# Performance work log

Hardware: AMD Instinct MI355X
Metric: run time of the kernel (lower is better)

The kernel has to match this reference:

```python
import jax, jax.numpy as jnp
import numpy as np

N_HEADS = 16
ROPE_BASE = 10000.0

def _rope_cos_sin(seq_len, head_dim):
    # freqs[t, j] = t / base**(2j/head_dim), j over head_dim//2 pairs
    inv_freq = 1.0 / (ROPE_BASE ** (jnp.arange(0, head_dim, 2, dtype=jnp.float32) / head_dim))
    t = jnp.arange(seq_len, dtype=jnp.float32)
    freqs = t[:, None] * inv_freq[None, :]          # [S, hd/2]
    return jnp.cos(freqs), jnp.sin(freqs)

def _apply_rope(x, cos, sin):
    # x: [B, S, H, hd]; pairs are interleaved (even, odd) -> complex (re, im)
    xr = x[..., 0::2]
    xi = x[..., 1::2]
    c = cos[None, :, None, :]
    s = sin[None, :, None, :]
    out_r = xr * c - xi * s
    out_i = xr * s + xi * c
    # interleave back: [..., hd/2, 2] -> [..., hd]
    return jnp.stack([out_r, out_i], axis=-1).reshape(x.shape)

def setup_inputs() -> dict:
    key = jax.random.key(0)
    ks = jax.random.split(key, 5)
    B, S, D = 2, 2048, 2048
    x = jax.random.normal(ks[0], (B, S, D), dtype=jnp.float32)
    w_scale = 0.02
    wq = jax.random.normal(ks[1], (D, D), dtype=jnp.float32) * w_scale
    wk = jax.random.normal(ks[2], (D, D), dtype=jnp.float32) * w_scale
    wv = jax.random.normal(ks[3], (D, D), dtype=jnp.float32) * w_scale
    wo = jax.random.normal(ks[4], (D, D), dtype=jnp.float32) * w_scale
    return {"x": x, "wq": wq, "wk": wk, "wv": wv, "wo": wo}

def reference(x, wq, wk, wv, wo):
    B, S, D = x.shape
    H = N_HEADS
    hd = D // H
    # QKV projections (torch Linear: y = x @ W^T)
    q = (x @ wq.T).reshape(B, S, H, hd)
    k = (x @ wk.T).reshape(B, S, H, hd)
    v = (x @ wv.T).reshape(B, S, H, hd)
    cos, sin = _rope_cos_sin(S, hd)
    q = _apply_rope(q, cos, sin)
    k = _apply_rope(k, cos, sin)
    # -> [B, H, S, hd]
    q = q.transpose(0, 2, 1, 3)
    k = k.transpose(0, 2, 1, 3)
    v = v.transpose(0, 2, 1, 3)
    scale = 1.0 / jnp.sqrt(jnp.float32(hd))
    scores = jnp.einsum('bhqd,bhkd->bhqk', q, k) * scale
    causal = jnp.tril(jnp.ones((S, S), dtype=bool))
    scores = jnp.where(causal[None, None], scores, jnp.float32(-1e30))
    probs = jax.nn.softmax(scores, axis=-1)
    attn = jnp.einsum('bhqk,bhkd->bhqd', probs, v)  # [B, H, S, hd]
    attn = attn.transpose(0, 2, 1, 3).reshape(B, S, D)
    return attn @ wo.T
```

## Files before the change

### kernel.cpp

```cpp
#include <hip/hip_runtime.h>
#include <hip/hip_bf16.h>

using bf16 = __hip_bfloat16;
typedef __attribute__((ext_vector_type(8))) short short8;
typedef __attribute__((ext_vector_type(4))) float floatx4;
typedef __attribute__((ext_vector_type(2))) float floatx2;

#define GLDS16(g, l)                                                        \
  __builtin_amdgcn_global_load_lds(                                         \
      (const __attribute__((address_space(1))) void*)(g),                   \
      (__attribute__((address_space(3))) void*)(l), 16, 0, 0)

#define MFMA16(a, b, c) __builtin_amdgcn_mfma_f32_16x16x32_bf16(a, b, c, 0, 0, 0)

__device__ __forceinline__ short f2b(float x) {
  union { bf16 h; short s; } u;
  u.h = __float2bfloat16(x);
  return u.s;
}
__device__ __forceinline__ void st(float* p, float v) { *p = v; }
__device__ __forceinline__ void st(bf16* p, float v) { *p = __float2bfloat16(v); }

template <int CTRL>
__device__ __forceinline__ float dpp_f(float x) {
  return __int_as_float(__builtin_amdgcn_update_dpp(
      0, __float_as_int(x), CTRL, 0xF, 0xF, true));
}
__device__ __forceinline__ float red16_max(float x) {
  x = fmaxf(x, dpp_f<0xB1>(x));
  x = fmaxf(x, dpp_f<0x4E>(x));
  x = fmaxf(x, dpp_f<0x141>(x));
  x = fmaxf(x, dpp_f<0x140>(x));
  return x;
}
__device__ __forceinline__ float red16_sum(float x) {
  x += dpp_f<0xB1>(x);
  x += dpp_f<0x4E>(x);
  x += dpp_f<0x141>(x);
  x += dpp_f<0x140>(x);
  return x;
}

__global__ void cast_kernel(const float* __restrict__ in, bf16* __restrict__ out,
                            long n) {
  long i = ((long)blockIdx.x * blockDim.x + threadIdx.x) * 8;
  if (i >= n) return;
  floatx4 a = *(const floatx4*)(in + i);
  floatx4 b = *(const floatx4*)(in + i + 4);
  short8 r;
  r[0] = f2b(a[0]); r[1] = f2b(a[1]); r[2] = f2b(a[2]); r[3] = f2b(a[3]);
  r[4] = f2b(b[0]); r[5] = f2b(b[1]); r[6] = f2b(b[2]); r[7] = f2b(b[3]);
  *(short8*)(out + i) = r;
}

__global__ void rope_tab_kernel(floatx2* __restrict__ tab) {
  const int t = blockIdx.x * blockDim.x + threadIdx.x;
  const int s = t >> 6, p = t & 63;
  const float invf = exp2f(-(float)p * (13.287712379549449f / 64.0f));
  float sn, cs;
  sincosf((float)s * invf, &sn, &cs);
  floatx2 e; e[0] = cs; e[1] = sn;
  tab[t] = e;
}

__device__ __forceinline__ void gemm_core(
    const bf16* __restrict__ A, const bf16* __restrict__ B, int K,
    long m0, long n0, bf16* As, bf16* Bs, floatx4 (&acc)[8][4])
{
  const int tid  = threadIdx.x;
  const int wave = tid >> 6;
  const int lane = tid & 63;
  const int quad = lane >> 4;
  const int l16  = lane & 15;
  const int wr = wave >> 1;
  const int wc = wave & 1;

  long ga[4];
  int aoff[4];
#pragma unroll
  for (int i = 0; i < 4; i++) {
    const int c = i * 256 + tid;
    const int row = c >> 2;
    const int gch = (c & 3) ^ ((c >> 3) & 3);
    ga[i] = (m0 + row) * (long)K + gch * 8;
    aoff[i] = (i * 256 + wave * 64) * 8;
  }
  long gb[2];
  int boff[2];
#pragma unroll
  for (int i = 0; i < 2; i++) {
    const int c = i * 256 + tid;
    const int row = c >> 2;
    const int gch = (c & 3) ^ ((c >> 3) & 3);
    gb[i] = (n0 + row) * (long)K + gch * 8;
    boff[i] = (i * 256 + wave * 64) * 8;
  }

  const int qs = (quad ^ ((l16 >> 1) & 3)) * 8;

#pragma unroll
  for (int mi = 0; mi < 8; mi++)
#pragma unroll
    for (int ni = 0; ni < 4; ni++) {
      floatx4 z = {0.f, 0.f, 0.f, 0.f};
      acc[mi][ni] = z;
    }

  const int NT = K >> 5;

#pragma unroll
  for (int t = 0; t < 2; t++) {
    bf16* Ad = As + t * 8192;
    bf16* Bd = Bs + t * 4096;
    const long kk = (long)t * 32;
#pragma unroll
    for (int i = 0; i < 4; i++) GLDS16(A + ga[i] + kk, Ad + aoff[i]);
#pragma unroll
    for (int i = 0; i < 2; i++) GLDS16(B + gb[i] + kk, Bd + boff[i]);
  }

  int sl = 0;
  for (int t = 0; t < NT; t++) {
    if (t < NT - 1) asm volatile("s_waitcnt vmcnt(6)" ::: "memory");
    else            asm volatile("s_waitcnt vmcnt(0)" ::: "memory");
    __builtin_amdgcn_s_barrier();

    const bf16* Ab = As + sl * 8192;
    const bf16* Bb = Bs + sl * 4096;

    short8 a[8], b[4];
#pragma unroll
    for (int mi = 0; mi < 8; mi++)
      a[mi] = *(const short8*)(Ab + (wr * 128 + mi * 16 + l16) * 32 + qs);
#pragma unroll
    for (int ni = 0; ni < 4; ni++)
      b[ni] = *(const short8*)(Bb + (wc * 64 + ni * 16 + l16) * 32 + qs);

    if (t + 2 < NT) {
      int s2 = sl + 2; if (s2 >= 3) s2 -= 3;
      bf16* Ad = As + s2 * 8192;
      bf16* Bd = Bs + s2 * 4096;
      const long kk = (long)(t + 2) * 32;
#pragma unroll
      for (int i = 0; i < 4; i++) GLDS16(A + ga[i] + kk, Ad + aoff[i]);
#pragma unroll
      for (int i = 0; i < 2; i++) GLDS16(B + gb[i] + kk, Bd + boff[i]);
    }

    asm volatile("s_waitcnt lgkmcnt(0)" ::: "memory");
    __builtin_amdgcn_sched_barrier(0);
    __builtin_amdgcn_s_setprio(1);
#pragma unroll
    for (int mi = 0; mi < 8; mi++)
#pragma unroll
      for (int ni = 0; ni < 4; ni++)
        acc[mi][ni] = MFMA16(a[mi], b[ni], acc[mi][ni]);
    __builtin_amdgcn_s_setprio(0);

    sl++; if (sl >= 3) sl = 0;
  }
}

__global__ __launch_bounds__(256, 2) void qkv_gemm(
    const bf16* __restrict__ A,
    const bf16* __restrict__ B0, const bf16* __restrict__ B1,
    const bf16* __restrict__ B2,
    bf16* __restrict__ C0, bf16* __restrict__ C1, bf16* __restrict__ Cvt,
    const floatx2* __restrict__ rtab,
    int M, int N, int K)
{
  __shared__ __align__(16) bf16 As[3 * 8192];
  __shared__ __align__(16) bf16 Bs[3 * 4096];

  const int sel = blockIdx.y >> 4;
  const long m0 = (long)blockIdx.x * 256;
  const long n0 = (long)(blockIdx.y & 15) * 128;
  const bf16* B = (sel == 0) ? B0 : ((sel == 1) ? B1 : B2);

  floatx4 acc[8][4];
  gemm_core(A, B, K, m0, n0, As, Bs, acc);

  const int tid  = threadIdx.x;
  const int wave = tid >> 6;
  const int lane = tid & 63;
  const int quad = lane >> 4;
  const int l16  = lane & 15;
  const int wr = wave >> 1;
  const int wc = wave & 1;

  if (sel < 2) {
    bf16* C = (sel == 0) ? C0 : C1;
    const float qscale = (sel == 0)
        ? (0.08838834764831845f * 1.4426950408889634f) : 1.0f;
    const float sgn = (l16 & 1) ? 1.0f : -1.0f;
#pragma unroll
    for (int ni = 0; ni < 4; ni++) {
      const int n = (int)n0 + wc * 64 + ni * 16 + l16;
      const int p = (n & 127) >> 1;
#pragma unroll
      for (int mi = 0; mi < 8; mi++) {
        floatx4 v = acc[mi][ni];
        const int mbase = (int)m0 + wr * 128 + mi * 16 + quad * 4;
#pragma unroll
        for (int r = 0; r < 4; r++) {
          const int spos = (mbase + r) & 2047;
          const floatx2 cssn = rtab[spos * 64 + p];
          const float pv = dpp_f<0xB1>(v[r]);
          const float outv = (v[r] * cssn[0] + pv * (sgn * cssn[1])) * qscale;
          st(&C[(long)(mbase + r) * N + n], outv);
        }
      }
    }
  } else {
#pragma unroll
    for (int ni = 0; ni < 4; ni++) {
      const int n = (int)n0 + wc * 64 + ni * 16 + l16;
      const int hh = n >> 7, d = n & 127;
#pragma unroll
      for (int mi = 0; mi < 8; mi++) {
        floatx4 v = acc[mi][ni];
        const int m = (int)m0 + wr * 128 + mi * 16 + quad * 4;
        const int bb = m >> 11, s = m & 2047;
        unsigned long long pk =
            (unsigned long long)(unsigned short)f2b(v[0]) |
            ((unsigned long long)(unsigned short)f2b(v[1]) << 16) |
            ((unsigned long long)(unsigned short)f2b(v[2]) << 32) |
            ((unsigned long long)(unsigned short)f2b(v[3]) << 48);
        *(unsigned long long*)(Cvt + ((long)((bb * 16 + hh) * 128 + d)) * 2048 + s) = pk;
      }
    }
  }
}

__global__ __launch_bounds__(256, 2) void gemm_out(
    const bf16* __restrict__ A, const bf16* __restrict__ B,
    float* __restrict__ C, int M, int N, int K)
{
  __shared__ __align__(16) bf16 As[3 * 8192];
  __shared__ __align__(16) bf16 Bs[3 * 4096];
  const long m0 = (long)blockIdx.x * 256;
  const long n0 = (long)blockIdx.y * 128;

  floatx4 acc[8][4];
  gemm_core(A, B, K, m0, n0, As, Bs, acc);

  const int tid  = threadIdx.x;
  const int wave = tid >> 6;
  const int lane = tid & 63;
  const int quad = lane >> 4;
  const int l16  = lane & 15;
  const int wr = wave >> 1;
  const int wc = wave & 1;

#pragma unroll
  for (int mi = 0; mi < 8; mi++)
#pragma unroll
    for (int ni = 0; ni < 4; ni++) {
      floatx4 v = acc[mi][ni];
      const long row = m0 + wr * 128 + mi * 16 + quad * 4;
      const long col = n0 + wc * 64 + ni * 16 + l16;
#pragma unroll
      for (int r = 0; r < 4; r++)
        C[(row + r) * (long)N + col] = v[r];
    }
}

#define NEG_BIG (-30000.0f)

__global__ __launch_bounds__(256) void flash_attn(
    const bf16* __restrict__ q, const bf16* __restrict__ k,
    const bf16* __restrict__ vt, bf16* __restrict__ o, int S)
{
  __shared__ bf16 Ks[64 * 136];
  __shared__ bf16 Vt[128 * 72];
  __shared__ bf16 Ps[4][32 * 72];

  const int tid  = threadIdx.x;
  const int wave = tid >> 6;
  const int lane = tid & 63;
  const int quad = lane >> 4;
  const int l16  = lane & 15;

  const int bh = blockIdx.x;
  const int b  = bh >> 4, h = bh & 15;
  const int q0 = ((int)gridDim.y - 1 - (int)blockIdx.y) * 128;

  const bf16* Qb = q + ((long)b * S * 16 + h) * 128;
  const bf16* Kb = k + ((long)b * S * 16 + h) * 128;
  const bf16* Vg = vt + (long)bh * 128 * S;
  bf16*       Ob = o + ((long)b * S * 16 + h) * 128;

  int kr[4], kc[4], vr[4], vc[4];
#pragma unroll
  for (int it = 0; it < 4; it++) {
    const int c = tid + it * 256;
    kr[it] = c >> 4;  kc[it] = (c & 15) * 8;
    vr[it] = c >> 3;  vc[it] = (c & 7) * 8;
  }

  short8 aq[2][4];
#pragma unroll
  for (int mi = 0; mi < 2; mi++)
#pragma unroll
    for (int kt = 0; kt < 4; kt++)
      aq[mi][kt] = *(const short8*)(
          Qb + (long)(q0 + wave * 32 + mi * 16 + l16) * 2048 + kt * 32 + quad * 8);

  float m_i[2][4], l_i[2][4];
  floatx4 oacc[2][8];
  const floatx4 zero4 = {0.f, 0.f, 0.f, 0.f};
#pragma unroll
  for (int mi = 0; mi < 2; mi++) {
#pragma unroll
    for (int r = 0; r < 4; r++) { m_i[mi][r] = NEG_BIG; l_i[mi][r] = 0.f; }
#pragma unroll
    for (int dt = 0; dt < 8; dt++) oacc[mi][dt] = zero4;
  }

  const int wrow0 = q0 + wave * 32;
  const int last  = q0 + 64;

  short8 kreg[4], vreg[4];
#pragma unroll
  for (int it = 0; it < 4; it++) {
    kreg[it] = *(const short8*)(Kb + (long)kr[it] * 2048 + kc[it]);
    vreg[it] = *(const short8*)(Vg + (long)vr[it] * S + vc[it]);
  }

  for (int kt0 = 0; kt0 <= last; kt0 += 64) {
    __syncthreads();

#pragma unroll
    for (int it = 0; it < 4; it++) {
      *(short8*)(Ks + kr[it] * 136 + kc[it]) = kreg[it];
      *(short8*)(Vt + vr[it] * 72 + vc[it]) = vreg[it];
    }
    __syncthreads();

    if (kt0 < last) {
      const int n0 = kt0 + 64;
#pragma unroll
      for (int it = 0; it < 4; it++) {
        kreg[it] = *(const short8*)(Kb + (long)(n0 + kr[it]) * 2048 + kc[it]);
        vreg[it] = *(const short8*)(Vg + (long)vr[it] * S + n0 + vc[it]);
      }
    }

    if (kt0 <= wrow0 + 31) {
      floatx4 sc[2][4];
#pragma unroll
      for (int mi = 0; mi < 2; mi++)
#pragma unroll
        for (int nt = 0; nt < 4; nt++) sc[mi][nt] = zero4;

      __builtin_amdgcn_s_setprio(1);
#pragma unroll
      for (int nt = 0; nt < 4; nt++)
#pragma unroll
        for (int kt = 0; kt < 4; kt++) {
          short8 bk = *(const short8*)(Ks + (nt * 16 + l16) * 136 + kt * 32 + quad * 8);
          sc[0][nt] = __builtin_amdgcn_mfma_f32_16x16x32_bf16(aq[0][kt], bk, sc[0][nt], 0, 0, 0);
          sc[1][nt] = __builtin_amdgcn_mfma_f32_16x16x32_bf16(aq[1][kt], bk, sc[1][nt], 0, 0, 0);
        }
      __builtin_amdgcn_s_setprio(0);

      const bool needmask = (kt0 + 63 > wrow0);
      float mx[2][4];
      int allskip = 1;
#pragma unroll
      for (int mi = 0; mi < 2; mi++) {
#pragma unroll
        for (int r = 0; r < 4; r++) {
          const int qr = wrow0 + mi * 16 + quad * 4 + r;
          float m = NEG_BIG;
          if (needmask) {
#pragma unroll
            for (int nt = 0; nt < 4; nt++) {
              const int kc2 = kt0 + nt * 16 + l16;
              float vsc = (kc2 <= qr) ? sc[mi][nt][r] : NEG_BIG;
              sc[mi][nt][r] = vsc;
              m = fmaxf(m, vsc);
            }
          } else {
#pragma unroll
            for (int nt = 0; nt < 4; nt++) m = fmaxf(m, sc[mi][nt][r]);
          }
          m = red16_max(m);
          mx[mi][r] = m;
          allskip &= (m <= m_i[mi][r] + 8.0f) ? 1 : 0;
        }
      }

      if (!__all(allskip)) {
#pragma unroll
        for (int mi = 0; mi < 2; mi++) {
#pragma unroll
          for (int r = 0; r < 4; r++) {
            const float mnew = fmaxf(m_i[mi][r], mx[mi][r]);
            const float alpha = exp2f(m_i[mi][r] - mnew);
            m_i[mi][r] = mnew;
            l_i[mi][r] *= alpha;
#pragma unroll
            for (int dt = 0; dt < 8; dt++) oacc[mi][dt][r] *= alpha;
          }
        }
      }

#pragma unroll
      for (int mi = 0; mi < 2; mi++) {
#pragma unroll
        for (int r = 0; r < 4; r++) {
          float rs = 0.f;
#pragma unroll
          for (int nt = 0; nt < 4; nt++) {
            float p = exp2f(sc[mi][nt][r] - m_i[mi][r]);
            sc[mi][nt][r] = p;
            rs += p;
          }
          rs = red16_sum(rs);
          l_i[mi][r] += rs;
        }
      }

#pragma unroll
      for (int mi = 0; mi < 2; mi++)
#pragma unroll
        for (int nt = 0; nt < 4; nt++)
#pragma unroll
          for (int r = 0; r < 4; r++)
            Ps[wave][(mi * 16 + quad * 4 + r) * 72 + nt * 16 + l16] =
                __float2bfloat16(sc[mi][nt][r]);

      __builtin_amdgcn_s_setprio(1);
#pragma unroll
      for (int ks = 0; ks < 2; ks++) {
        short8 ap0 = *(const short8*)(&Ps[wave][(l16) * 72 + ks * 32 + quad * 8]);
        short8 ap1 = *(const short8*)(&Ps[wave][(16 + l16) * 72 + ks * 32 + quad * 8]);
#pragma unroll
        for (int dt = 0; dt < 8; dt++) {
          short8 bv = *(const short8*)(Vt + (dt * 16 + l16) * 72 + ks * 32 + quad * 8);
          oacc[0][dt] = __builtin_amdgcn_mfma_f32_16x16x32_bf16(ap0, bv, oacc[0][dt], 0, 0, 0);
          oacc[1][dt] = __builtin_amdgcn_mfma_f32_16x16x32_bf16(ap1, bv, oacc[1][dt], 0, 0, 0);
        }
      }
      __builtin_amdgcn_s_setprio(0);
    }
  }

#pragma unroll
  for (int mi = 0; mi < 2; mi++)
#pragma unroll
    for (int r = 0; r < 4; r++) {
      const float inv = 1.0f / l_i[mi][r];
      const long s = q0 + wave * 32 + mi * 16 + quad * 4 + r;
#pragma unroll
      for (int dt = 0; dt < 8; dt++)
        Ob[s * 2048 + dt * 16 + l16] = __float2bfloat16(oacc[mi][dt][r] * inv);
    }
}

extern "C" void kernel_launch(void* const* d_in, const int* in_sizes, int n_in,
                              void* d_out, int out_size, void* d_ws, size_t ws_size,
                              hipStream_t stream) {
  const float* x  = (const float*)d_in[0];
  const float* wq = (const float*)d_in[1];
  const float* wk = (const float*)d_in[2];
  const float* wv = (const float*)d_in[3];
  const float* wo = (const float*)d_in[4];
  float* out = (float*)d_out;

  const int B = 2, S = 2048, D = 2048, H = 16;
  const int M = B * S;
  const long tsz = (long)M * D;
  const long wsz = (long)D * D;

  if (ws_size < 4 * (size_t)tsz * sizeof(bf16)) return;

  bf16* qb  = (bf16*)d_ws;
  bf16* kb  = qb + tsz;
  bf16* vtb = kb + tsz;
  bf16* ab  = vtb + tsz;

  bf16* xb  = (bf16*)d_out;
  bf16* wqb = xb + tsz;
  bf16* wkb = wqb + wsz;
  bf16* wvb = ab;
  floatx2* rtab = (floatx2*)(ab + wsz);
  bf16* wob = qb;

  cast_kernel<<<(int)(tsz / 8 / 256), 256, 0, stream>>>(x,  xb,  tsz);
  cast_kernel<<<(int)(wsz / 8 / 256), 256, 0, stream>>>(wq, wqb, wsz);
  cast_kernel<<<(int)(wsz / 8 / 256), 256, 0, stream>>>(wk, wkb, wsz);
  cast_kernel<<<(int)(wsz / 8 / 256), 256, 0, stream>>>(wv, wvb, wsz);
  rope_tab_kernel<<<(S * 64) / 256, 256, 0, stream>>>(rtab);

  qkv_gemm<<<dim3(16, 48), 256, 0, stream>>>(
      xb, wqb, wkb, wvb, qb, kb, vtb, rtab, M, D, D);

  flash_attn<<<dim3(B * H, S / 128), 256, 0, stream>>>(qb, kb, vtb, ab, S);

  cast_kernel<<<(int)(wsz / 8 / 256), 256, 0, stream>>>(wo, wob, wsz);
  gemm_out<<<dim3(16, 16), 256, 0, stream>>>(ab, wob, out, M, D, D);
}
```

Before: 417.3 us.

## Fuse pre-casts and rope table into one launch; drop LDS staging in attention

```diff
diff --git a/kernel.cpp b/kernel.cpp
--- a/kernel.cpp
+++ b/kernel.cpp
@@ -39,6 +39,45 @@
   x += dpp_f<0x141>(x);
   x += dpp_f<0x140>(x);
   return x;
+}
+
+__global__ void fused_pre(const float* __restrict__ x,
+                          const float* __restrict__ wq,
+                          const float* __restrict__ wk,
+                          const float* __restrict__ wv,
+                          bf16* __restrict__ xb, bf16* __restrict__ wqb,
+                          bf16* __restrict__ wkb, bf16* __restrict__ wvb,
+                          floatx2* __restrict__ rtab, long wsz) {
+  const int slice = blockIdx.y;
+  if (slice == 5) {
+    const int t = blockIdx.x * blockDim.x + threadIdx.x;
+    if (t < 131072) {
+      const int s = t >> 6, p = t & 63;
+      const float invf = exp2f(-(float)p * (13.287712379549449f / 64.0f));
+      float sn, cs;
+      sincosf((float)s * invf, &sn, &cs);
+      floatx2 e; e[0] = cs; e[1] = sn;
+      rtab[t] = e;
+    }
+    return;
+  }
+  const float* src;
+  bf16* dst;
+  switch (slice) {
+    case 0:  src = x;        dst = xb;        break;
+    case 1:  src = x + wsz;  dst = xb + wsz;  break;
+    case 2:  src = wq;       dst = wqb;       break;
+    case 3:  src = wk;       dst = wkb;       break;
+    default: src = wv;       dst = wvb;       break;
+  }
+  const long i = ((long)blockIdx.x * blockDim.x + threadIdx.x) * 8;
+  if (i >= wsz) return;
+  floatx4 a = *(const floatx4*)(src + i);
+  floatx4 b = *(const floatx4*)(src + i + 4);
+  short8 r;
+  r[0] = f2b(a[0]); r[1] = f2b(a[1]); r[2] = f2b(a[2]); r[3] = f2b(a[3]);
+  r[4] = f2b(b[0]); r[5] = f2b(b[1]); r[6] = f2b(b[2]); r[7] = f2b(b[3]);
+  *(short8*)(dst + i) = r;
 }
 
 __global__ void cast_kernel(const float* __restrict__ in, bf16* __restrict__ out,
@@ -51,16 +90,6 @@
   r[0] = f2b(a[0]); r[1] = f2b(a[1]); r[2] = f2b(a[2]); r[3] = f2b(a[3]);
   r[4] = f2b(b[0]); r[5] = f2b(b[1]); r[6] = f2b(b[2]); r[7] = f2b(b[3]);
   *(short8*)(out + i) = r;
-}
-
-__global__ void rope_tab_kernel(floatx2* __restrict__ tab) {
-  const int t = blockIdx.x * blockDim.x + threadIdx.x;
-  const int s = t >> 6, p = t & 63;
-  const float invf = exp2f(-(float)p * (13.287712379549449f / 64.0f));
-  float sn, cs;
-  sincosf((float)s * invf, &sn, &cs);
-  floatx2 e; e[0] = cs; e[1] = sn;
-  tab[t] = e;
 }
 
 __device__ __forceinline__ void gemm_core(
@@ -271,8 +300,6 @@
     const bf16* __restrict__ q, const bf16* __restrict__ k,
     const bf16* __restrict__ vt, bf16* __restrict__ o, int S)
 {
-  __shared__ bf16 Ks[64 * 136];
-  __shared__ bf16 Vt[128 * 72];
   __shared__ bf16 Ps[4][32 * 72];
 
   const int tid  = threadIdx.x;
@@ -290,14 +317,6 @@
   const bf16* Vg = vt + (long)bh * 128 * S;
   bf16*       Ob = o + ((long)b * S * 16 + h) * 128;
 
-  int kr[4], kc[4], vr[4], vc[4];
-#pragma unroll
-  for (int it = 0; it < 4; it++) {
-    const int c = tid + it * 256;
-    kr[it] = c >> 4;  kc[it] = (c & 15) * 8;
-    vr[it] = c >> 3;  vc[it] = (c & 7) * 8;
-  }
-
   short8 aq[2][4];
 #pragma unroll
   for (int mi = 0; mi < 2; mi++)
@@ -318,133 +337,108 @@
   }
 
   const int wrow0 = q0 + wave * 32;
-  const int last  = q0 + 64;
-
-  short8 kreg[4], vreg[4];
-#pragma unroll
-  for (int it = 0; it < 4; it++) {
-    kreg[it] = *(const short8*)(Kb + (long)kr[it] * 2048 + kc[it]);
-    vreg[it] = *(const short8*)(Vg + (long)vr[it] * S + vc[it]);
-  }
-
-  for (int kt0 = 0; kt0 <= last; kt0 += 64) {
-    __syncthreads();
-
-#pragma unroll
-    for (int it = 0; it < 4; it++) {
-      *(short8*)(Ks + kr[it] * 136 + kc[it]) = kreg[it];
-      *(short8*)(Vt + vr[it] * 72 + vc[it]) = vreg[it];
-    }
-    __syncthreads();
-
-    if (kt0 < last) {
-      const int n0 = kt0 + 64;
-#pragma unroll
-      for (int it = 0; it < 4; it++) {
-        kreg[it] = *(const short8*)(Kb + (long)(n0 + kr[it]) * 2048 + kc[it]);
-        vreg[it] = *(const short8*)(Vg + (long)vr[it] * S + n0 + vc[it]);
-      }
-    }
-
-    if (kt0 <= wrow0 + 31) {
-      floatx4 sc[2][4];
-#pragma unroll
-      for (int mi = 0; mi < 2; mi++)
-#pragma unroll
-        for (int nt = 0; nt < 4; nt++) sc[mi][nt] = zero4;
-
-      __builtin_amdgcn_s_setprio(1);
+  const int wlast = wrow0 + 31;
+
+  for (int kt0 = 0; kt0 <= wlast; kt0 += 64) {
+    floatx4 sc[2][4];
+#pragma unroll
+    for (int mi = 0; mi < 2; mi++)
+#pragma unroll
+      for (int nt = 0; nt < 4; nt++) sc[mi][nt] = zero4;
+
+    __builtin_amdgcn_s_setprio(1);
+#pragma unroll
+    for (int nt = 0; nt < 4; nt++)
+#pragma unroll
+      for (int kt = 0; kt < 4; kt++) {
+        short8 bk = *(const short8*)(
+            Kb + (long)(kt0 + nt * 16 + l16) * 2048 + kt * 32 + quad * 8);
+        sc[0][nt] = __builtin_amdgcn_mfma_f32_16x16x32_bf16(aq[0][kt], bk, sc[0][nt], 0, 0, 0);
+        sc[1][nt] = __builtin_amdgcn_mfma_f32_16x16x32_bf16(aq[1][kt], bk, sc[1][nt], 0, 0, 0);
+      }
+    __builtin_amdgcn_s_setprio(0);
+
+    const bool needmask = (kt0 + 63 > wrow0);
+    float mx[2][4];
+    int allskip = 1;
+#pragma unroll
+    for (int mi = 0; mi < 2; mi++) {
+#pragma unroll
+      for (int r = 0; r < 4; r++) {
+        const int qr = wrow0 + mi * 16 + quad * 4 + r;
+        float m = NEG_BIG;
+        if (needmask) {
+#pragma unroll
+          for (int nt = 0; nt < 4; nt++) {
+            const int kc2 = kt0 + nt * 16 + l16;
+            float vsc = (kc2 <= qr) ? sc[mi][nt][r] : NEG_BIG;
+            sc[mi][nt][r] = vsc;
+            m = fmaxf(m, vsc);
+          }
+        } else {
+#pragma unroll
+          for (int nt = 0; nt < 4; nt++) m = fmaxf(m, sc[mi][nt][r]);
+        }
+        m = red16_max(m);
+        mx[mi][r] = m;
+        allskip &= (m <= m_i[mi][r] + 8.0f) ? 1 : 0;
+      }
+    }
+
+    if (!__all(allskip)) {
+#pragma unroll
+      for (int mi = 0; mi < 2; mi++) {
+#pragma unroll
+        for (int r = 0; r < 4; r++) {
+          const float mnew = fmaxf(m_i[mi][r], mx[mi][r]);
+          const float alpha = exp2f(m_i[mi][r] - mnew);
+          m_i[mi][r] = mnew;
+          l_i[mi][r] *= alpha;
+#pragma unroll
+          for (int dt = 0; dt < 8; dt++) oacc[mi][dt][r] *= alpha;
+        }
+      }
+    }
+
+#pragma unroll
+    for (int mi = 0; mi < 2; mi++) {
+#pragma unroll
+      for (int r = 0; r < 4; r++) {
+        float rs = 0.f;
+#pragma unroll
+        for (int nt = 0; nt < 4; nt++) {
+          float p = exp2f(sc[mi][nt][r] - m_i[mi][r]);
+          sc[mi][nt][r] = p;
+          rs += p;
+        }
+        rs = red16_sum(rs);
+        l_i[mi][r] += rs;
+      }
+    }
+
+#pragma unroll
+    for (int mi = 0; mi < 2; mi++)
 #pragma unroll
       for (int nt = 0; nt < 4; nt++)
 #pragma unroll
-        for (int kt = 0; kt < 4; kt++) {
-          short8 bk = *(const short8*)(Ks + (nt * 16 + l16) * 136 + kt * 32 + quad * 8);
-          sc[0][nt] = __builtin_amdgcn_mfma_f32_16x16x32_bf16(aq[0][kt], bk, sc[0][nt], 0, 0, 0);
-          sc[1][nt] = __builtin_amdgcn_mfma_f32_16x16x32_bf16(aq[1][kt], bk, sc[1][nt], 0, 0, 0);
-        }
-      __builtin_amdgcn_s_setprio(0);
-
-      const bool needmask = (kt0 + 63 > wrow0);
-      float mx[2][4];
-      int allskip = 1;
-#pragma unroll
-      for (int mi = 0; mi < 2; mi++) {
-#pragma unroll
-        for (int r = 0; r < 4; r++) {
-          const int qr = wrow0 + mi * 16 + quad * 4 + r;
-          float m = NEG_BIG;
-          if (needmask) {
-#pragma unroll
-            for (int nt = 0; nt < 4; nt++) {
-              const int kc2 = kt0 + nt * 16 + l16;
-              float vsc = (kc2 <= qr) ? sc[mi][nt][r] : NEG_BIG;
-              sc[mi][nt][r] = vsc;
-              m = fmaxf(m, vsc);
-            }
-          } else {
-#pragma unroll
-            for (int nt = 0; nt < 4; nt++) m = fmaxf(m, sc[mi][nt][r]);
-          }
-          m = red16_max(m);
-          mx[mi][r] = m;
-          allskip &= (m <= m_i[mi][r] + 8.0f) ? 1 : 0;
-        }
-      }
-
-      if (!__all(allskip)) {
-#pragma unroll
-        for (int mi = 0; mi < 2; mi++) {
-#pragma unroll
-          for (int r = 0; r < 4; r++) {
-            const float mnew = fmaxf(m_i[mi][r], mx[mi][r]);
-            const float alpha = exp2f(m_i[mi][r] - mnew);
-            m_i[mi][r] = mnew;
-            l_i[mi][r] *= alpha;
-#pragma unroll
-            for (int dt = 0; dt < 8; dt++) oacc[mi][dt][r] *= alpha;
-          }
-        }
-      }
-
-#pragma unroll
-      for (int mi = 0; mi < 2; mi++) {
-#pragma unroll
-        for (int r = 0; r < 4; r++) {
-          float rs = 0.f;
-#pragma unroll
-          for (int nt = 0; nt < 4; nt++) {
-            float p = exp2f(sc[mi][nt][r] - m_i[mi][r]);
-            sc[mi][nt][r] = p;
-            rs += p;
-          }
-          rs = red16_sum(rs);
-          l_i[mi][r] += rs;
-        }
-      }
-
-#pragma unroll
-      for (int mi = 0; mi < 2; mi++)
-#pragma unroll
-        for (int nt = 0; nt < 4; nt++)
-#pragma unroll
-          for (int r = 0; r < 4; r++)
-            Ps[wave][(mi * 16 + quad * 4 + r) * 72 + nt * 16 + l16] =
-                __float2bfloat16(sc[mi][nt][r]);
-
-      __builtin_amdgcn_s_setprio(1);
-#pragma unroll
-      for (int ks = 0; ks < 2; ks++) {
-        short8 ap0 = *(const short8*)(&Ps[wave][(l16) * 72 + ks * 32 + quad * 8]);
-        short8 ap1 = *(const short8*)(&Ps[wave][(16 + l16) * 72 + ks * 32 + quad * 8]);
-#pragma unroll
-        for (int dt = 0; dt < 8; dt++) {
-          short8 bv = *(const short8*)(Vt + (dt * 16 + l16) * 72 + ks * 32 + quad * 8);
-          oacc[0][dt] = __builtin_amdgcn_mfma_f32_16x16x32_bf16(ap0, bv, oacc[0][dt], 0, 0, 0);
-          oacc[1][dt] = __builtin_amdgcn_mfma_f32_16x16x32_bf16(ap1, bv, oacc[1][dt], 0, 0, 0);
-        }
-      }
-      __builtin_amdgcn_s_setprio(0);
-    }
+        for (int r = 0; r < 4; r++)
+          Ps[wave][(mi * 16 + quad * 4 + r) * 72 + nt * 16 + l16] =
+              __float2bfloat16(sc[mi][nt][r]);
+
+    __builtin_amdgcn_s_setprio(1);
+#pragma unroll
+    for (int ks = 0; ks < 2; ks++) {
+      short8 ap0 = *(const short8*)(&Ps[wave][(l16) * 72 + ks * 32 + quad * 8]);
+      short8 ap1 = *(const short8*)(&Ps[wave][(16 + l16) * 72 + ks * 32 + quad * 8]);
+#pragma unroll
+      for (int dt = 0; dt < 8; dt++) {
+        short8 bv = *(const short8*)(
+            Vg + (long)(dt * 16 + l16) * S + kt0 + ks * 32 + quad * 8);
+        oacc[0][dt] = __builtin_amdgcn_mfma_f32_16x16x32_bf16(ap0, bv, oacc[0][dt], 0, 0, 0);
+        oacc[1][dt] = __builtin_amdgcn_mfma_f32_16x16x32_bf16(ap1, bv, oacc[1][dt], 0, 0, 0);
+      }
+    }
+    __builtin_amdgcn_s_setprio(0);
   }
 
 #pragma unroll
@@ -488,11 +482,8 @@
   floatx2* rtab = (floatx2*)(ab + wsz);
   bf16* wob = qb;
 
-  cast_kernel<<<(int)(tsz / 8 / 256), 256, 0, stream>>>(x,  xb,  tsz);
-  cast_kernel<<<(int)(wsz / 8 / 256), 256, 0, stream>>>(wq, wqb, wsz);
-  cast_kernel<<<(int)(wsz / 8 / 256), 256, 0, stream>>>(wk, wkb, wsz);
-  cast_kernel<<<(int)(wsz / 8 / 256), 256, 0, stream>>>(wv, wvb, wsz);
-  rope_tab_kernel<<<(S * 64) / 256, 256, 0, stream>>>(rtab);
+  fused_pre<<<dim3((int)(wsz / 8 / 256), 6), 256, 0, stream>>>(
+      x, wq, wk, wv, xb, wqb, wkb, wvb, rtab, wsz);
 
   qkv_gemm<<<dim3(16, 48), 256, 0, stream>>>(
       xb, wqb, wkb, wvb, qb, kb, vtb, rtab, M, D, D);
```

Result: slower. 513.2 us (+23.0%).

## Fuse input casts and rope table into one launch; shrink output GEMM tile to 128x128

Applied to the files above, without the earlier changes.

```diff
diff --git a/kernel.cpp b/kernel.cpp
--- a/kernel.cpp
+++ b/kernel.cpp
@@ -39,6 +39,45 @@
   x += dpp_f<0x141>(x);
   x += dpp_f<0x140>(x);
   return x;
+}
+
+__global__ void fused_pre(const float* __restrict__ x,
+                          const float* __restrict__ wq,
+                          const float* __restrict__ wk,
+                          const float* __restrict__ wv,
+                          bf16* __restrict__ xb, bf16* __restrict__ wqb,
+                          bf16* __restrict__ wkb, bf16* __restrict__ wvb,
+                          floatx2* __restrict__ rtab, long wsz) {
+  const int slice = blockIdx.y;
+  if (slice == 5) {
+    const int t = blockIdx.x * blockDim.x + threadIdx.x;
+    if (t < 131072) {
+      const int s = t >> 6, p = t & 63;
+      const float invf = exp2f(-(float)p * (13.287712379549449f / 64.0f));
+      float sn, cs;
+      sincosf((float)s * invf, &sn, &cs);
+      floatx2 e; e[0] = cs; e[1] = sn;
+      rtab[t] = e;
+    }
+    return;
+  }
+  const float* src;
+  bf16* dst;
+  switch (slice) {
+    case 0:  src = x;        dst = xb;        break;
+    case 1:  src = x + wsz;  dst = xb + wsz;  break;
+    case 2:  src = wq;       dst = wqb;       break;
+    case 3:  src = wk;       dst = wkb;       break;
+    default: src = wv;       dst = wvb;       break;
+  }
+  const long i = ((long)blockIdx.x * blockDim.x + threadIdx.x) * 8;
+  if (i >= wsz) return;
+  floatx4 a = *(const floatx4*)(src + i);
+  floatx4 b = *(const floatx4*)(src + i + 4);
+  short8 r;
+  r[0] = f2b(a[0]); r[1] = f2b(a[1]); r[2] = f2b(a[2]); r[3] = f2b(a[3]);
+  r[4] = f2b(b[0]); r[5] = f2b(b[1]); r[6] = f2b(b[2]); r[7] = f2b(b[3]);
+  *(short8*)(dst + i) = r;
 }
 
 __global__ void cast_kernel(const float* __restrict__ in, bf16* __restrict__ out,
@@ -51,16 +90,6 @@
   r[0] = f2b(a[0]); r[1] = f2b(a[1]); r[2] = f2b(a[2]); r[3] = f2b(a[3]);
   r[4] = f2b(b[0]); r[5] = f2b(b[1]); r[6] = f2b(b[2]); r[7] = f2b(b[3]);
   *(short8*)(out + i) = r;
-}
-
-__global__ void rope_tab_kernel(floatx2* __restrict__ tab) {
-  const int t = blockIdx.x * blockDim.x + threadIdx.x;
-  const int s = t >> 6, p = t & 63;
-  const float invf = exp2f(-(float)p * (13.287712379549449f / 64.0f));
-  float sn, cs;
-  sincosf((float)s * invf, &sn, &cs);
-  floatx2 e; e[0] = cs; e[1] = sn;
-  tab[t] = e;
 }
 
 __device__ __forceinline__ void gemm_core(
@@ -161,6 +190,95 @@
   }
 }
 
+__device__ __forceinline__ void gemm_core128(
+    const bf16* __restrict__ A, const bf16* __restrict__ B, int K,
+    long m0, long n0, bf16* As, bf16* Bs, floatx4 (&acc)[4][4])
+{
+  const int tid  = threadIdx.x;
+  const int wave = tid >> 6;
+  const int lane = tid & 63;
+  const int quad = lane >> 4;
+  const int l16  = lane & 15;
+  const int wr = wave >> 1;
+  const int wc = wave & 1;
+
+  long ga[2], gb[2];
+  int soff[2];
+#pragma unroll
+  for (int i = 0; i < 2; i++) {
+    const int c = i * 256 + tid;
+    const int row = c >> 2;
+    const int gch = (c & 3) ^ ((c >> 3) & 3);
+    ga[i] = (m0 + row) * (long)K + gch * 8;
+    gb[i] = (n0 + row) * (long)K + gch * 8;
+    soff[i] = (i * 256 + wave * 64) * 8;
+  }
+
+  const int qs = (quad ^ ((l16 >> 1) & 3)) * 8;
+
+#pragma unroll
+  for (int mi = 0; mi < 4; mi++)
+#pragma unroll
+    for (int ni = 0; ni < 4; ni++) {
+      floatx4 z = {0.f, 0.f, 0.f, 0.f};
+      acc[mi][ni] = z;
+    }
+
+  const int NT = K >> 5;
+
+#pragma unroll
+  for (int t = 0; t < 2; t++) {
+    bf16* Ad = As + t * 4096;
+    bf16* Bd = Bs + t * 4096;
+    const long kk = (long)t * 32;
+#pragma unroll
+    for (int i = 0; i < 2; i++) GLDS16(A + ga[i] + kk, Ad + soff[i]);
+#pragma unroll
+    for (int i = 0; i < 2; i++) GLDS16(B + gb[i] + kk, Bd + soff[i]);
+  }
+
+  int sl = 0;
+  for (int t = 0; t < NT; t++) {
+    if (t < NT - 1) asm volatile("s_waitcnt vmcnt(4)" ::: "memory");
+    else            asm volatile("s_waitcnt vmcnt(0)" ::: "memory");
+    __builtin_amdgcn_s_barrier();
+
+    const bf16* Ab = As + sl * 4096;
+    const bf16* Bb = Bs + sl * 4096;
+
+    short8 a[4], b[4];
+#pragma unroll
+    for (int mi = 0; mi < 4; mi++)
+      a[mi] = *(const short8*)(Ab + (wr * 64 + mi * 16 + l16) * 32 + qs);
+#pragma unroll
+    for (int ni = 0; ni < 4; ni++)
+      b[ni] = *(const short8*)(Bb + (wc * 64 + ni * 16 + l16) * 32 + qs);
+
+    if (t + 2 < NT) {
+      int s2 = sl + 2; if (s2 >= 3) s2 -= 3;
+      bf16* Ad = As + s2 * 4096;
+      bf16* Bd = Bs + s2 * 4096;
+      const long kk = (long)(t + 2) * 32;
+#pragma unroll
+      for (int i = 0; i < 2; i++) GLDS16(A + ga[i] + kk, Ad + soff[i]);
+#pragma unroll
+      for (int i = 0; i < 2; i++) GLDS16(B + gb[i] + kk, Bd + soff[i]);
+    }
+
+    asm volatile("s_waitcnt lgkmcnt(0)" ::: "memory");
+    __builtin_amdgcn_sched_barrier(0);
+    __builtin_amdgcn_s_setprio(1);
+#pragma unroll
+    for (int mi = 0; mi < 4; mi++)
+#pragma unroll
+      for (int ni = 0; ni < 4; ni++)
+        acc[mi][ni] = MFMA16(a[mi], b[ni], acc[mi][ni]);
+    __builtin_amdgcn_s_setprio(0);
+
+    sl++; if (sl >= 3) sl = 0;
+  }
+}
+
 __global__ __launch_bounds__(256, 2) void qkv_gemm(
     const bf16* __restrict__ A,
     const bf16* __restrict__ B0, const bf16* __restrict__ B1,
@@ -236,13 +354,13 @@
     const bf16* __restrict__ A, const bf16* __restrict__ B,
     float* __restrict__ C, int M, int N, int K)
 {
-  __shared__ __align__(16) bf16 As[3 * 8192];
+  __shared__ __align__(16) bf16 As[3 * 4096];
   __shared__ __align__(16) bf16 Bs[3 * 4096];
-  const long m0 = (long)blockIdx.x * 256;
+  const long m0 = (long)blockIdx.x * 128;
   const long n0 = (long)blockIdx.y * 128;
 
-  floatx4 acc[8][4];
-  gemm_core(A, B, K, m0, n0, As, Bs, acc);
+  floatx4 acc[4][4];
+  gemm_core128(A, B, K, m0, n0, As, Bs, acc);
 
   const int tid  = threadIdx.x;
   const int wave = tid >> 6;
@@ -253,11 +371,11 @@
   const int wc = wave & 1;
 
 #pragma unroll
-  for (int mi = 0; mi < 8; mi++)
+  for (int mi = 0; mi < 4; mi++)
 #pragma unroll
     for (int ni = 0; ni < 4; ni++) {
       floatx4 v = acc[mi][ni];
-      const long row = m0 + wr * 128 + mi * 16 + quad * 4;
+      const long row = m0 + wr * 64 + mi * 16 + quad * 4;
       const long col = n0 + wc * 64 + ni * 16 + l16;
 #pragma unroll
       for (int r = 0; r < 4; r++)
@@ -488,11 +606,8 @@
   floatx2* rtab = (floatx2*)(ab + wsz);
   bf16* wob = qb;
 
-  cast_kernel<<<(int)(tsz / 8 / 256), 256, 0, stream>>>(x,  xb,  tsz);
-  cast_kernel<<<(int)(wsz / 8 / 256), 256, 0, stream>>>(wq, wqb, wsz);
-  cast_kernel<<<(int)(wsz / 8 / 256), 256, 0, stream>>>(wk, wkb, wsz);
-  cast_kernel<<<(int)(wsz / 8 / 256), 256, 0, stream>>>(wv, wvb, wsz);
-  rope_tab_kernel<<<(S * 64) / 256, 256, 0, stream>>>(rtab);
+  fused_pre<<<dim3((int)(wsz / 8 / 256), 6), 256, 0, stream>>>(
+      x, wq, wk, wv, xb, wqb, wkb, wvb, rtab, wsz);
 
   qkv_gemm<<<dim3(16, 48), 256, 0, stream>>>(
       xb, wqb, wkb, wvb, qb, kb, vtb, rtab, M, D, D);
@@ -500,5 +615,5 @@
   flash_attn<<<dim3(B * H, S / 128), 256, 0, stream>>>(qb, kb, vtb, ab, S);
 
   cast_kernel<<<(int)(wsz / 8 / 256), 256, 0, stream>>>(wo, wob, wsz);
-  gemm_out<<<dim3(16, 16), 256, 0, stream>>>(ab, wob, out, M, D, D);
-}
+  gemm_out<<<dim3(32, 16), 256, 0, stream>>>(ab, wob, out, M, D, D);
+}
```

Measured after the change: 410.8 us. Within noise of the previous version (-1.5%).
